# Kernel tuning notes

Measured on AMD Instinct MI355X. Metric: run time of the kernel, lower is better.

## Reference

```python
import jax, jax.numpy as jnp
import numpy as np

C, U, V, D, B = 5, 6144, 6144, 64, 4096  # classes, users, items, feat dim, batch pairs


def setup_inputs() -> dict:
    key = jax.random.key(0)
    ks = jax.random.split(key, 16)
    s = 1.0 / np.sqrt(D)
    adj = (jax.random.uniform(ks[0], (C, U, V)) < 0.01).astype(jnp.float32)
    return {
        "u": jax.random.randint(ks[1], (B,), 0, U),
        "v": jax.random.randint(ks[2], (B,), 0, V),
        "u_emb": jax.random.normal(ks[3], (U, D), jnp.float32) * 0.1,
        "v_emb": jax.random.normal(ks[4], (V, D), jnp.float32) * 0.1,
        "W1u": jax.random.normal(ks[5], (C, D, D), jnp.float32) * s,
        "b1u": jnp.zeros((C, D), jnp.float32),
        "W1v": jax.random.normal(ks[6], (C, D, D), jnp.float32) * s,
        "b1v": jnp.zeros((C, D), jnp.float32),
        "W2u": jax.random.normal(ks[7], (C, D, D), jnp.float32) * s,
        "b2u": jnp.zeros((C, D), jnp.float32),
        "W2v": jax.random.normal(ks[8], (C, D, D), jnp.float32) * s,
        "b2v": jnp.zeros((C, D), jnp.float32),
        "Q": jax.random.normal(ks[9], (C, D, D), jnp.float32) * s,
        "adj": adj,
    }


def reference(u, v, u_emb, v_emb, W1u, b1u, W1v, b1v, W2u, b2u, W2v, b2v, Q, adj):
    # ---- layer 1: per-class graph convolution, summed over rating classes ----
    # user codes aggregate item features through adj_c; item codes through adj_c^T
    msg_v = jnp.einsum("vd,cde->cve", v_emb, W1v)            # [C,V,D]
    h_u = jax.nn.relu(jnp.einsum("cuv,cve->ue", adj, msg_v) + b1v.sum(0))  # [U,D]
    msg_u = jnp.einsum("ud,cde->cue", u_emb, W1u)            # [C,U,D]
    h_v = jax.nn.relu(jnp.einsum("cuv,cue->ve", adj, msg_u) + b1u.sum(0))  # [V,D]
    # ---- layer 2 ----
    z_u = jnp.einsum("cuv,cve->ue", adj, jnp.einsum("vd,cde->cve", h_v, W2u)) + b2u.sum(0)
    z_v = jnp.einsum("cuv,cue->ve", adj, jnp.einsum("ud,cde->cue", h_u, W2v)) + b2v.sum(0)
    # ---- bilinear decoder over batch of (user, item) pairs ----
    zu = z_u[u]                                              # [B,D] gather
    zv = z_v[v]                                              # [B,D] gather
    logits = jnp.einsum("bd,cde,be->bc", zu, Q, zv)          # [B,C] per-class rating logits
    return logits
```

## Files before the change

kernel.cpp:

```cpp
#include <hip/hip_runtime.h>

#define NC   5
#define NU   6144
#define NV   6144
#define ND   64
#define NB   4096
#define CAP  128
#define NW   192
#define HALF (NC * NU)

__device__ __forceinline__ unsigned int spread4(unsigned int x) {
  x &= 0xFFu;
  x = (x | (x << 12)) & 0x000F000Fu;
  x = (x | (x << 6))  & 0x03030303u;
  x = (x | (x << 3))  & 0x11111111u;
  return x;
}

__global__ __launch_bounds__(256) void k_bitmask(
    const float* __restrict__ adj,
    unsigned int* __restrict__ maskT) {
  __shared__ unsigned int rowwords[64][9];
  const int b = blockIdx.x;
  const int c  = b / 2304;
  const int rem = b - c * 2304;
  const int tu = rem / 24;
  const int tv = rem - tu * 24;
  const int wave = threadIdx.x >> 6;
  const int lane = threadIdx.x & 63;

  float4 av[16];
  {
    const float* base = adj +
        ((size_t)(c * NU + tu * 64 + wave * 16) * NV + tv * 256);
    #pragma unroll
    for (int rr = 0; rr < 16; ++rr)
      av[rr] = ((const float4*)(base + (size_t)rr * NV))[lane];
  }
  #pragma unroll
  for (int rr = 0; rr < 16; ++rr) {
    const unsigned long long b0 = __ballot(av[rr].x != 0.0f);
    const unsigned long long b1 = __ballot(av[rr].y != 0.0f);
    const unsigned long long b2 = __ballot(av[rr].z != 0.0f);
    const unsigned long long b3 = __ballot(av[rr].w != 0.0f);
    if (lane < 8) {
      const unsigned int e0 = spread4((unsigned int)(b0 >> (lane * 8)));
      const unsigned int e1 = spread4((unsigned int)(b1 >> (lane * 8)));
      const unsigned int e2 = spread4((unsigned int)(b2 >> (lane * 8)));
      const unsigned int e3 = spread4((unsigned int)(b3 >> (lane * 8)));
      rowwords[wave * 16 + rr][lane] = e0 | (e1 << 1) | (e2 << 2) | (e3 << 3);
    }
  }
  __syncthreads();

  {
    const int k  = threadIdx.x >> 5;
    const int rb = threadIdx.x & 31;
    unsigned int* p = maskT + ((size_t)c * 192 + tv * 8 + k) * 6144 + tu * 64;
    p[rb]      = rowwords[rb][k];
    p[rb + 32] = rowwords[rb + 32][k];
  }

  {
    const int j = threadIdx.x;
    const int w = j >> 5, bit = j & 31;
    unsigned int w0 = 0, w1 = 0;
    #pragma unroll
    for (int r = 0; r < 32; ++r) {
      w0 |= ((rowwords[r][w]      >> bit) & 1u) << r;
      w1 |= ((rowwords[r + 32][w] >> bit) & 1u) << r;
    }
    unsigned int* p = maskT +
        ((size_t)(NC + c) * 192 + tu * 2) * 6144 + tv * 256 + j;
    p[0]    = w0;
    p[6144] = w1;
  }
}

__global__ __launch_bounds__(256) void k_expand(
    const unsigned int* __restrict__ maskT,
    int* __restrict__ cnt,
    unsigned short* __restrict__ idx) {
  const int wv = blockIdx.x * 4 + (threadIdx.x >> 6);
  const int lane = threadIdx.x & 63;
  const int sc = wv / 96;
  const int g  = wv - sc * 96;
  const int dim = g * 64 + lane;
  const unsigned int* base = maskT + (size_t)sc * 192 * 6144 + dim;
  const int R = sc * 6144 + dim;
  unsigned short* orow = idx + (size_t)R * CAP;
  int cur = 0;
  for (int wb = 0; wb < NW; wb += 16) {
    unsigned int wreg[16];
    #pragma unroll
    for (int t = 0; t < 16; ++t)
      wreg[t] = base[(size_t)(wb + t) * 6144];
    #pragma unroll
    for (int t = 0; t < 16; ++t) {
      unsigned int m = wreg[t];
      const int wbase = (wb + t) * 32;
      while (m) {
        const int bb = __ffs(m) - 1;
        if (cur < CAP) orow[cur] = (unsigned short)(wbase + bb);
        ++cur;
        m &= m - 1;
      }
    }
  }
  cnt[R] = cur < CAP ? cur : CAP;
}

__global__ __launch_bounds__(256) void k_gather(
    const int* __restrict__ cnt,
    const unsigned short* __restrict__ idx,
    const float* __restrict__ tabA,
    const float* __restrict__ tabB,
    float* __restrict__ agg) {
  __shared__ float4 red4[4][16];
  const int wave = threadIdx.x >> 6;
  const int lane = threadIdx.x & 63;
  const int R = blockIdx.x * 4 + wave;
  const int g    = lane >> 4;
  const int e16  = lane & 15;
  int n = cnt[R];
  n = n > CAP ? CAP : n;
  const unsigned short* l = idx + (size_t)R * CAP;
  const float4* tab = (const float4*)(R < HALF ? tabA : tabB);
  float4 a0 = make_float4(0.f,0.f,0.f,0.f), a1 = a0, a2 = a0, a3 = a0;
  int i = 0;
  for (; i + 16 <= n; i += 16) {
    const int j0 = l[i + g], j1 = l[i + 4 + g];
    const int j2 = l[i + 8 + g], j3 = l[i + 12 + g];
    const float4 x0 = tab[j0 * 16 + e16];
    const float4 x1 = tab[j1 * 16 + e16];
    const float4 x2 = tab[j2 * 16 + e16];
    const float4 x3 = tab[j3 * 16 + e16];
    a0.x += x0.x; a0.y += x0.y; a0.z += x0.z; a0.w += x0.w;
    a1.x += x1.x; a1.y += x1.y; a1.z += x1.z; a1.w += x1.w;
    a2.x += x2.x; a2.y += x2.y; a2.z += x2.z; a2.w += x2.w;
    a3.x += x3.x; a3.y += x3.y; a3.z += x3.z; a3.w += x3.w;
  }
  for (; i + 4 <= n; i += 4) {
    const float4 x = tab[(int)l[i + g] * 16 + e16];
    a0.x += x.x; a0.y += x.y; a0.z += x.z; a0.w += x.w;
  }
  if (i + g < n) {
    const float4 x = tab[(int)l[i + g] * 16 + e16];
    a1.x += x.x; a1.y += x.y; a1.z += x.z; a1.w += x.w;
  }
  a0.x += a1.x + a2.x + a3.x;
  a0.y += a1.y + a2.y + a3.y;
  a0.z += a1.z + a2.z + a3.z;
  a0.w += a1.w + a2.w + a3.w;
  #pragma unroll
  for (int off = 16; off < 64; off <<= 1) {
    a0.x += __shfl_xor(a0.x, off, 64);
    a0.y += __shfl_xor(a0.y, off, 64);
    a0.z += __shfl_xor(a0.z, off, 64);
    a0.w += __shfl_xor(a0.w, off, 64);
  }
  if (g == 0) red4[wave][e16] = a0;
  __syncthreads();
  if (g == 0) ((float4*)agg)[(size_t)R * 16 + e16] = red4[wave][e16];
}

__global__ __launch_bounds__(256) void k_gemm5(
    const float* __restrict__ agg,
    const float* __restrict__ Wa, const float* __restrict__ ba,
    float* __restrict__ outA,
    const float* __restrict__ Wb, const float* __restrict__ bb,
    float* __restrict__ outB,
    int do_relu) {
  const int half = blockIdx.x >= 384;
  const float* W    = half ? Wb : Wa;
  const float* bias = half ? bb : ba;
  float* out        = half ? outB : outA;
  const float* aggh = agg + (size_t)half * HALF * 64;
  const int lane = threadIdx.x & 63;
  const int wave = threadIdx.x >> 6;
  const int r0 = (blockIdx.x - half * 384) * 16 + wave * 4;
  float bs = 0.0f;
  #pragma unroll
  for (int c = 0; c < NC; ++c) bs += bias[c * 64 + lane];
  float acc[4] = {bs, bs, bs, bs};
  for (int c = 0; c < NC; ++c) {
    float w[64];
    #pragma unroll
    for (int d = 0; d < 64; ++d) w[d] = W[c * 4096 + d * 64 + lane];
    #pragma unroll
    for (int r = 0; r < 4; ++r) {
      const float4* ar = (const float4*)(aggh + ((size_t)c * 6144 + r0 + r) * 64);
      #pragma unroll
      for (int d4 = 0; d4 < 16; ++d4) {
        const float4 a = ar[d4];
        acc[r] = fmaf(a.x, w[d4 * 4 + 0], acc[r]);
        acc[r] = fmaf(a.y, w[d4 * 4 + 1], acc[r]);
        acc[r] = fmaf(a.z, w[d4 * 4 + 2], acc[r]);
        acc[r] = fmaf(a.w, w[d4 * 4 + 3], acc[r]);
      }
    }
  }
  #pragma unroll
  for (int r = 0; r < 4; ++r) {
    const float x = do_relu ? fmaxf(acc[r], 0.0f) : acc[r];
    out[(size_t)(r0 + r) * 64 + lane] = x;
  }
}

__global__ __launch_bounds__(256) void k_decoder(
    const int* __restrict__ uu, const int* __restrict__ vv,
    const float* __restrict__ z_u, const float* __restrict__ z_v,
    const float* __restrict__ Q,
    float* __restrict__ out) {
  const int lane = threadIdx.x & 63;
  const int wave = threadIdx.x >> 6;
  const int b = blockIdx.x * 4 + wave;
  const int ub = uu[b];
  const int vb = vv[b];
  const float zve = z_v[(size_t)vb * 64 + lane];
  const float* zu = z_u + (size_t)ub * 64;
  #pragma unroll
  for (int c = 0; c < NC; ++c) {
    const float* Qc = Q + c * 64 * 64;
    float t = 0.0f;
    #pragma unroll
    for (int d = 0; d < 64; ++d) t = fmaf(zu[d], Qc[d * 64 + lane], t);
    float p = t * zve;
    #pragma unroll
    for (int off = 32; off > 0; off >>= 1) p += __shfl_xor(p, off, 64);
    if (lane == 0) out[(size_t)b * NC + c] = p;
  }
}

extern "C" void kernel_launch(void* const* d_in, const int* in_sizes, int n_in,
                              void* d_out, int out_size, void* d_ws, size_t ws_size,
                              hipStream_t stream) {
  const int*   u     = (const int*)d_in[0];
  const int*   v     = (const int*)d_in[1];
  const float* u_emb = (const float*)d_in[2];
  const float* v_emb = (const float*)d_in[3];
  const float* W1u   = (const float*)d_in[4];
  const float* b1u   = (const float*)d_in[5];
  const float* W1v   = (const float*)d_in[6];
  const float* b1v   = (const float*)d_in[7];
  const float* W2u   = (const float*)d_in[8];
  const float* b2u   = (const float*)d_in[9];
  const float* W2v   = (const float*)d_in[10];
  const float* b2v   = (const float*)d_in[11];
  const float* Q     = (const float*)d_in[12];
  const float* adj   = (const float*)d_in[13];
  float* out = (float*)d_out;

  char* ws = (char*)d_ws;
  int* cnt = (int*)ws;
  unsigned short* idxL = (unsigned short*)(ws + 245760);
  char* maskbase = ws + 245760 + 15728640;
  unsigned int* maskT = (unsigned int*)maskbase;
  float* agg = (float*)maskbase;
  float* h_u = (float*)(maskbase + 15728640);
  float* h_v = (float*)(maskbase + 17301504);
  float* z_u = (float*)(maskbase + 18874368);
  float* z_v = (float*)(maskbase + 20447232);

  k_bitmask<<<NC * 96 * 24, 256, 0, stream>>>(adj, maskT);
  k_expand<<<240, 256, 0, stream>>>(maskT, cnt, idxL);

  k_gather<<<2 * HALF / 4, 256, 0, stream>>>(cnt, idxL, v_emb, u_emb, agg);
  k_gemm5<<<768, 256, 0, stream>>>(agg, W1v, b1v, h_u, W1u, b1u, h_v, 1);
  k_gather<<<2 * HALF / 4, 256, 0, stream>>>(cnt, idxL, h_v, h_u, agg);
  k_gemm5<<<768, 256, 0, stream>>>(agg, W2u, b2u, z_u, W2v, b2v, z_v, 0);
  k_decoder<<<NB / 4, 256, 0, stream>>>(u, v, z_u, z_v, Q, out);
}
```

Before: 1.232 ms.

## Fuse adjacency bitmask and index expansion into one kernel with atomic row counters

```diff
diff --git a/kernel.cpp b/kernel.cpp
--- a/kernel.cpp
+++ b/kernel.cpp
@@ -6,7 +6,6 @@
 #define ND   64
 #define NB   4096
 #define CAP  128
-#define NW   192
 #define HALF (NC * NU)
 
 __device__ __forceinline__ unsigned int spread4(unsigned int x) {
@@ -17,9 +16,10 @@
   return x;
 }
 
-__global__ __launch_bounds__(256) void k_bitmask(
+__global__ __launch_bounds__(256) void k_adj2idx(
     const float* __restrict__ adj,
-    unsigned int* __restrict__ maskT) {
+    int* __restrict__ cnt,
+    unsigned short* __restrict__ idx) {
   __shared__ unsigned int rowwords[64][9];
   const int b = blockIdx.x;
   const int c  = b / 2304;
@@ -53,12 +53,35 @@
   }
   __syncthreads();
 
-  {
-    const int k  = threadIdx.x >> 5;
-    const int rb = threadIdx.x & 31;
-    unsigned int* p = maskT + ((size_t)c * 192 + tv * 8 + k) * 6144 + tu * 64;
-    p[rb]      = rowwords[rb][k];
-    p[rb + 32] = rowwords[rb + 32][k];
+  #pragma unroll
+  for (int p = 0; p < 2; ++p) {
+    const int rloc = lane >> 3;
+    const int wloc = lane & 7;
+    const int r = wave * 16 + p * 8 + rloc;
+    const unsigned int wbits = rowwords[r][wloc];
+    const int pc = __popc(wbits);
+    int pre = pc;
+    #pragma unroll
+    for (int d = 1; d < 8; d <<= 1) {
+      const int y = __shfl_up(pre, d, 64);
+      if (wloc >= d) pre += y;
+    }
+    const int total = __shfl(pre, rloc * 8 + 7, 64);
+    const int excl  = pre - pc;
+    const int R = c * 6144 + tu * 64 + r;
+    int base = 0;
+    if (wloc == 0 && total > 0) base = atomicAdd(&cnt[R], total);
+    base = __shfl(base, rloc * 8, 64);
+    unsigned int m = wbits;
+    int o = base + excl;
+    unsigned short* orow = idx + (size_t)R * CAP;
+    const int vbase = tv * 256 + wloc * 32;
+    while (m) {
+      const int bb = __ffs(m) - 1;
+      if (o < CAP) orow[o] = (unsigned short)(vbase + bb);
+      ++o;
+      m &= m - 1;
+    }
   }
 
   {
@@ -70,44 +93,28 @@
       w0 |= ((rowwords[r][w]      >> bit) & 1u) << r;
       w1 |= ((rowwords[r + 32][w] >> bit) & 1u) << r;
     }
-    unsigned int* p = maskT +
-        ((size_t)(NC + c) * 192 + tu * 2) * 6144 + tv * 256 + j;
-    p[0]    = w0;
-    p[6144] = w1;
-  }
-}
-
-__global__ __launch_bounds__(256) void k_expand(
-    const unsigned int* __restrict__ maskT,
-    int* __restrict__ cnt,
-    unsigned short* __restrict__ idx) {
-  const int wv = blockIdx.x * 4 + (threadIdx.x >> 6);
-  const int lane = threadIdx.x & 63;
-  const int sc = wv / 96;
-  const int g  = wv - sc * 96;
-  const int dim = g * 64 + lane;
-  const unsigned int* base = maskT + (size_t)sc * 192 * 6144 + dim;
-  const int R = sc * 6144 + dim;
-  unsigned short* orow = idx + (size_t)R * CAP;
-  int cur = 0;
-  for (int wb = 0; wb < NW; wb += 16) {
-    unsigned int wreg[16];
-    #pragma unroll
-    for (int t = 0; t < 16; ++t)
-      wreg[t] = base[(size_t)(wb + t) * 6144];
-    #pragma unroll
-    for (int t = 0; t < 16; ++t) {
-      unsigned int m = wreg[t];
-      const int wbase = (wb + t) * 32;
+    const int cj = __popc(w0) + __popc(w1);
+    if (cj > 0) {
+      const int R = (NC + c) * 6144 + tv * 256 + j;
+      int o = atomicAdd(&cnt[R], cj);
+      unsigned short* orow = idx + (size_t)R * CAP;
+      const int ubase = tu * 64;
+      unsigned int m = w0;
       while (m) {
         const int bb = __ffs(m) - 1;
-        if (cur < CAP) orow[cur] = (unsigned short)(wbase + bb);
-        ++cur;
+        if (o < CAP) orow[o] = (unsigned short)(ubase + bb);
+        ++o;
         m &= m - 1;
       }
-    }
-  }
-  cnt[R] = cur < CAP ? cur : CAP;
+      m = w1;
+      while (m) {
+        const int bb = __ffs(m) - 1;
+        if (o < CAP) orow[o] = (unsigned short)(ubase + 32 + bb);
+        ++o;
+        m &= m - 1;
+      }
+    }
+  }
 }
 
 __global__ __launch_bounds__(256) void k_gather(
@@ -254,16 +261,16 @@
   char* ws = (char*)d_ws;
   int* cnt = (int*)ws;
   unsigned short* idxL = (unsigned short*)(ws + 245760);
-  char* maskbase = ws + 245760 + 15728640;
-  unsigned int* maskT = (unsigned int*)maskbase;
-  float* agg = (float*)maskbase;
-  float* h_u = (float*)(maskbase + 15728640);
-  float* h_v = (float*)(maskbase + 17301504);
-  float* z_u = (float*)(maskbase + 18874368);
-  float* z_v = (float*)(maskbase + 20447232);
-
-  k_bitmask<<<NC * 96 * 24, 256, 0, stream>>>(adj, maskT);
-  k_expand<<<240, 256, 0, stream>>>(maskT, cnt, idxL);
+  char* fbase = ws + 245760 + 15728640;
+  float* agg = (float*)fbase;
+  float* h_u = (float*)(fbase + 15728640);
+  float* h_v = (float*)(fbase + 17301504);
+  float* z_u = (float*)(fbase + 18874368);
+  float* z_v = (float*)(fbase + 20447232);
+
+  hipMemsetAsync(cnt, 0, 2 * NC * 6144 * sizeof(int), stream);
+
+  k_adj2idx<<<NC * 96 * 24, 256, 0, stream>>>(adj, cnt, idxL);
 
   k_gather<<<2 * HALF / 4, 256, 0, stream>>>(cnt, idxL, v_emb, u_emb, agg);
   k_gemm5<<<768, 256, 0, stream>>>(agg, W1v, b1v, h_u, W1u, b1u, h_v, 1);
```

After: 1.171 ms. 1.05x faster.
